# Kernel optimization log

Hardware: AMD Instinct MI355X
Metric: run time of the kernel (lower is better)

## Reference

```python
import jax, jax.numpy as jnp
import numpy as np

EPS = 1e-5
NUM_HEADS = 8
KEY_DIM = 32
V_DIM = 128  # att_ratio * key_dim

def bn2d(x, g, b, m, v):
    # inference BatchNorm2d on NCHW
    s = g * jax.lax.rsqrt(v + EPS)
    return x * s[None, :, None, None] + (b - m * s)[None, :, None, None]

def conv1x1(x, w):
    # w: [out_c, in_c], x: [B,C,H,W]
    return jnp.einsum('oc,bchw->bohw', w, x)

def _bn_params(key, c):
    k1, k2, k3, k4 = jax.random.split(key, 4)
    g = jax.random.uniform(k1, (c,), jnp.float32, 0.5, 1.5)
    b = jax.random.normal(k2, (c,), jnp.float32) * 0.1
    m = jax.random.normal(k3, (c,), jnp.float32) * 0.1
    v = jax.random.uniform(k4, (c,), jnp.float32, 0.5, 1.5)
    return g, b, m, v

def setup_inputs() -> dict:
    key = jax.random.key(0)
    ks = jax.random.split(key, 12)
    inp_dim, out_dim = 256, 512
    kv_out = (KEY_DIM + V_DIM) * NUM_HEADS      # 1280
    q_out = KEY_DIM * NUM_HEADS                 # 256
    merge_dim = V_DIM * NUM_HEADS               # 1024
    hid = out_dim * 2                            # mlp_ratio=2 -> 1024
    d = {}
    d['x'] = jax.random.normal(ks[0], (32, inp_dim, 32, 32), jnp.float32)
    d['kv_w'] = jax.random.normal(ks[1], (kv_out, inp_dim), jnp.float32) * 0.02
    d['kv_g'], d['kv_b'], d['kv_m'], d['kv_v'] = _bn_params(ks[2], kv_out)
    d['q_w'] = jax.random.normal(ks[3], (q_out, inp_dim), jnp.float32) * 0.02
    d['q_g'], d['q_b'], d['q_m'], d['q_v'] = _bn_params(ks[4], q_out)
    d['mg_w'] = jax.random.normal(ks[5], (out_dim, merge_dim), jnp.float32) * 0.02
    d['mg_g'], d['mg_b'], d['mg_m'], d['mg_v'] = _bn_params(ks[6], out_dim)
    d['fc1_w'] = jax.random.normal(ks[7], (hid, out_dim), jnp.float32) * 0.02
    d['bn1_g'], d['bn1_b'], d['bn1_m'], d['bn1_v'] = _bn_params(ks[8], hid)
    d['fc2_w'] = jax.random.normal(ks[9], (out_dim, hid), jnp.float32) * 0.02
    d['bn2_g'], d['bn2_b'], d['bn2_m'], d['bn2_v'] = _bn_params(ks[10], out_dim)
    return d

def reference(x, kv_w, kv_g, kv_b, kv_m, kv_v, q_w, q_g, q_b, q_m, q_v,
              mg_w, mg_g, mg_b, mg_m, mg_v,
              fc1_w, bn1_g, bn1_b, bn1_m, bn1_v,
              fc2_w, bn2_g, bn2_b, bn2_m, bn2_v):
    B, C, H, W = x.shape
    scale = KEY_DIM ** (-0.5)
    # kv projection: conv1x1 + BN, then split per head into k, v
    kv = bn2d(conv1x1(x, kv_w), kv_g, kv_b, kv_m, kv_v)
    kv = kv.reshape(B, NUM_HEADS, KEY_DIM + V_DIM, H * W)
    k = kv[:, :, :KEY_DIM]   # [B,h,Dk,N]
    v = kv[:, :, KEY_DIM:]   # [B,h,Dv,N]
    # query subsampling: AvgPool2d(kernel=1, stride=2) == strided slice
    xq = x[:, :, ::2, ::2]
    q = bn2d(conv1x1(xq, q_w), q_g, q_b, q_m, q_v)
    q = q.reshape(B, NUM_HEADS, KEY_DIM, -1)  # [B,h,Dk,Nq]
    # att = q^T @ k * scale, softmax over keys
    att = jax.nn.softmax(jnp.einsum('bhdq,bhdn->bhqn', q, k) * scale, axis=-1)
    h2, w2 = (H + 1) // 2, (W + 1) // 2
    # out = v @ att^T, channel-first layout
    o = jnp.einsum('bhvn,bhqn->bhvq', v, att).reshape(B, NUM_HEADS * V_DIM, h2, w2)
    # merge: GELU -> conv1x1 -> BN
    o = bn2d(conv1x1(jax.nn.gelu(o, approximate=False), mg_w), mg_g, mg_b, mg_m, mg_v)
    # ConvMlp: conv1x1 -> BN -> GELU -> conv1x1 -> BN
    y = bn2d(conv1x1(o, fc1_w), bn1_g, bn1_b, bn1_m, bn1_v)
    y = jax.nn.gelu(y, approximate=False)
    y = bn2d(conv1x1(y, fc2_w), bn2_g, bn2_b, bn2_m, bn2_v)
    return y
```

## Files before the change

kernel.cpp:

```cpp
#include <hip/hip_runtime.h>
#include <hip/hip_bf16.h>

#define BN_EPS 1e-5f

typedef short s8v __attribute__((ext_vector_type(8)));
typedef float f4v __attribute__((ext_vector_type(4)));
typedef unsigned short u16x8 __attribute__((ext_vector_type(8)));

__device__ __forceinline__ float bu2f(unsigned short u) {
    union { unsigned int i; float f; } c; c.i = ((unsigned int)u) << 16; return c.f;
}
__device__ __forceinline__ unsigned short f2bu(float f) {
    union { float f; unsigned int i; } c; c.f = f;
    unsigned int i = c.i;
    i += 0x7FFFu + ((i >> 16) & 1u);
    return (unsigned short)(i >> 16);
}
__device__ __forceinline__ float gelu_exact(float x) {
    return 0.5f * x * (1.0f + erff(x * 0.70710678118654752f));
}
__device__ __forceinline__ float ldin(const void* p, long i, bool f32) {
    return f32 ? ((const float*)p)[i] : bu2f(((const unsigned short*)p)[i]);
}
__device__ __forceinline__ s8v ldfrag(const unsigned short* p) {
    return *reinterpret_cast<const s8v*>(p);
}
__device__ __forceinline__ void gld16(const void* g, void* l) {
    __builtin_amdgcn_global_load_lds(
        (const __attribute__((address_space(1))) unsigned int*)g,
        (__attribute__((address_space(3))) unsigned int*)l, 16, 0, 0);
}
__device__ __forceinline__ s8v ldsw32(const unsigned short* T, int row, int quad) {
    return *reinterpret_cast<const s8v*>(T + row * 32 + ((quad ^ ((row >> 1) & 3)) << 3));
}
__device__ __forceinline__ s8v ldsw64(const unsigned short* T, int row, int chunk) {
    return *reinterpret_cast<const s8v*>(T + row * 64 + ((chunk ^ (row & 7)) << 3));
}
__device__ __forceinline__ int detect_f32(const unsigned short* xu) {
    int insane = 0;
    for (int i = 0; i < 128; ++i) {
        unsigned int e = (xu[i] >> 7) & 0xFFu;
        if (e == 255u || (e != 0u && (e < 96u || e > 159u))) ++insane;
    }
    return (insane >= 16) ? 1 : 0;
}

__global__ __launch_bounds__(256)
void prep_kernel(const void* __restrict__ x,
                 const void* __restrict__ w0, const void* __restrict__ w1,
                 const void* __restrict__ w2, const void* __restrict__ w3,
                 const void* __restrict__ w4,
                 unsigned short* __restrict__ wdst,
                 unsigned short* __restrict__ xT,
                 unsigned short* __restrict__ xqT,
                 int* __restrict__ dtf)
{
    __shared__ int sflag;
    __shared__ unsigned short T[64][66];
    const int tid = threadIdx.x;
    const int bid = blockIdx.x;
    if (tid == 0) {
        int fl = detect_f32((const unsigned short*)x);
        sflag = fl;
        if (bid == 0) *dtf = fl;
    }
    __syncthreads();
    const bool f = (sflag != 0);

    if (bid < 960) {
        long idx = (long)bid * 2048 + tid * 8;
        const void* s; long off;
        if (idx < 65536L) {
            long rk = idx >> 8;
            s = w0; off = ((rk >> 5) * 160 + (rk & 31)) * 256 + (idx & 255);
        } else if (idx < 327680L) {
            long rv = (idx - 65536L) >> 8;
            s = w0; off = ((rv >> 7) * 160 + 32 + (rv & 127)) * 256 + (idx & 255);
        }
        else if (idx <  393216L) { s = w1; off = idx - 327680L; }
        else if (idx <  917504L) { s = w2; off = idx - 393216L; }
        else if (idx < 1441792L) { s = w3; off = idx - 917504L; }
        else                     { s = w4; off = idx - 1441792L; }
        u16x8 pk;
        if (f) {
            float4 a = *((const float4*)((const float*)s + off));
            float4 b = *((const float4*)((const float*)s + off + 4));
            pk[0]=f2bu(a.x); pk[1]=f2bu(a.y); pk[2]=f2bu(a.z); pk[3]=f2bu(a.w);
            pk[4]=f2bu(b.x); pk[5]=f2bu(b.y); pk[6]=f2bu(b.z); pk[7]=f2bu(b.w);
        } else {
            pk = *((const u16x8*)((const unsigned short*)s + off));
        }
        *reinterpret_cast<u16x8*>(wdst + idx) = pk;
        return;
    }
    int b, c0, n0, ND; bool SUBS;
    if (bid < 3008) { int t = bid - 960;  b = t >> 6; int r = t & 63;
                      c0 = (r >> 4) * 64; n0 = (r & 15) * 64; ND = 1024; SUBS = false; }
    else            { int t = bid - 3008; b = t >> 4; int r = t & 15;
                      c0 = (r >> 2) * 64; n0 = (r & 3) * 64;  ND = 256;  SUBS = true; }
    unsigned short* dst = SUBS ? xqT : xT;
    {
        int nn = tid & 63, cq = tid >> 6;
        int n = n0 + nn;
        int sc = SUBS ? ((n >> 4) * 64 + (n & 15) * 2) : n;
        long base = ((long)b * 256 + c0 + cq * 16) * 1024 + sc;
        #pragma unroll
        for (int i = 0; i < 16; ++i)
            T[nn][cq * 16 + i] = f2bu(ldin(x, base + (long)i * 1024, f));
    }
    __syncthreads();
    {
        int cc = tid & 63, nq = tid >> 6;
        #pragma unroll
        for (int i = 0; i < 16; ++i) {
            int nn = nq * 16 + i;
            dst[((long)b * ND + n0 + nn) * 256 + c0 + cc] = T[nn][cc];
        }
    }
}

template<int OUT_MODE, bool DO_GELU, bool PRESCALE, bool REMAPK>
__global__ __launch_bounds__(256, 4)
void mfma_gemm(const unsigned short* __restrict__ A,
               const unsigned short* __restrict__ B,
               const void* __restrict__ gg, const void* __restrict__ bb,
               const void* __restrict__ mmu, const void* __restrict__ vv,
               void* __restrict__ out0,
               int M, int K, int N, const int* __restrict__ dtflag)
{
    __shared__ union {
        struct { unsigned short As[64 * 64]; unsigned short Bs[128 * 64]; } s;
        unsigned short tile[128 * 68];
    } u;
    __shared__ float sS[64], sO[64];

    const bool wf = (*dtflag != 0);
    const int tid = threadIdx.x;
    const int lane = tid & 63;
    const int wave = tid >> 6;
    const int quad = lane >> 4;
    const int l15  = lane & 15;
    const int wn2 = wave * 32;
    const int b  = blockIdx.z;
    const int bm = blockIdx.y * 64;
    const int bn = blockIdx.x * 128;

    if (tid < 64) {
        int m = bm + tid;
        int mo = REMAPK ? ((m >> 5) * 160 + (m & 31)) : m;
        float g  = ldin(gg,  mo, wf), be = ldin(bb,  mo, wf);
        float mu = ldin(mmu, mo, wf), va = ldin(vv,  mo, wf);
        float s = g * rsqrtf(va + BN_EPS);
        float o = be - mu * s;
        if (PRESCALE) { s *= 0.17677669529663687f; o *= 0.17677669529663687f; }
        sS[tid] = s; sO[tid] = o;
    }

    const unsigned short* Bb = B + (long)b * N * K;

    f4v acc[4][2];
    #pragma unroll
    for (int i = 0; i < 4; ++i)
        #pragma unroll
        for (int j = 0; j < 2; ++j) acc[i][j] = (f4v){0.f, 0.f, 0.f, 0.f};

    const int lr8 = lane >> 3;
    const int lc8 = lane & 7;

    for (int k0 = 0; k0 < K; k0 += 64) {
        #pragma unroll
        for (int j = 0; j < 2; ++j) {
            int base = wave * 16 + j * 8;
            int r = base + lr8;
            gld16(A + (long)(bm + r) * K + k0 + ((lc8 ^ (r & 7)) << 3),
                  u.s.As + base * 64);
        }
        #pragma unroll
        for (int j = 0; j < 4; ++j) {
            int base = wave * 32 + j * 8;
            int r = base + lr8;
            gld16(Bb + (long)(bn + r) * K + k0 + ((lc8 ^ (r & 7)) << 3),
                  u.s.Bs + base * 64);
        }
        __syncthreads();

        #pragma unroll
        for (int sk = 0; sk < 2; ++sk) {
            s8v af[4], bfr[2];
            #pragma unroll
            for (int i = 0; i < 4; ++i)
                af[i]  = ldsw64(u.s.As, i * 16 + l15, sk * 4 + quad);
            #pragma unroll
            for (int j = 0; j < 2; ++j)
                bfr[j] = ldsw64(u.s.Bs, wn2 + j * 16 + l15, sk * 4 + quad);
            #pragma unroll
            for (int i = 0; i < 4; ++i)
                #pragma unroll
                for (int j = 0; j < 2; ++j)
                    acc[i][j] = __builtin_amdgcn_mfma_f32_16x16x32_bf16(
                        af[i], bfr[j], acc[i][j], 0, 0, 0);
        }
        __syncthreads();
    }

    if (OUT_MODE == 0 || OUT_MODE == 3) {
        #pragma unroll
        for (int j = 0; j < 2; ++j) {
            int n = wn2 + j * 16 + l15;
            #pragma unroll
            for (int i = 0; i < 4; ++i) {
                int mcol = i * 16 + quad * 4;
                ushort4 pk;
                float v0 = acc[i][j][0] * sS[mcol + 0] + sO[mcol + 0];
                float v1 = acc[i][j][1] * sS[mcol + 1] + sO[mcol + 1];
                float v2 = acc[i][j][2] * sS[mcol + 2] + sO[mcol + 2];
                float v3 = acc[i][j][3] * sS[mcol + 3] + sO[mcol + 3];
                if (DO_GELU) {
                    v0 = gelu_exact(v0); v1 = gelu_exact(v1);
                    v2 = gelu_exact(v2); v3 = gelu_exact(v3);
                }
                pk.x = f2bu(v0); pk.y = f2bu(v1); pk.z = f2bu(v2); pk.w = f2bu(v3);
                *reinterpret_cast<ushort4*>(&u.tile[n * 68 + mcol]) = pk;
            }
        }
        __syncthreads();
        #pragma unroll
        for (int p = 0; p < 4; ++p) {
            int n = p * 32 + (tid >> 3), c = tid & 7;
            u16x8 val = *reinterpret_cast<const u16x8*>(&u.tile[n * 68 + c * 8]);
            if (OUT_MODE == 0) {
                *reinterpret_cast<u16x8*>(
                    (unsigned short*)out0 + ((long)b * N + bn + n) * M + bm + c * 8) = val;
            } else {
                int m = bm + c * 8, h = m >> 5;
                *reinterpret_cast<u16x8*>(
                    (unsigned short*)out0 + (((long)b * 8 + h) * N + bn + n) * 32 + (m & 31)) = val;
            }
        }
    } else {
        #pragma unroll
        for (int i = 0; i < 4; ++i) {
            int m0l = i * 16 + quad * 4;
            int m0  = bm + m0l;
            float s0 = sS[m0l + 0], o0 = sO[m0l + 0];
            float s1 = sS[m0l + 1], o1 = sO[m0l + 1];
            float s2 = sS[m0l + 2], o2 = sO[m0l + 2];
            float s3 = sS[m0l + 3], o3 = sO[m0l + 3];
            #pragma unroll
            for (int j = 0; j < 2; ++j) {
                int n = bn + wn2 + j * 16 + l15;
                float v0 = acc[i][j][0] * s0 + o0;
                float v1 = acc[i][j][1] * s1 + o1;
                float v2 = acc[i][j][2] * s2 + o2;
                float v3 = acc[i][j][3] * s3 + o3;
                int b2 = n >> 8, nl = n & 255;
                long ob = ((long)b2 * M + m0) * 256 + nl;
                if (wf) {
                    ((float*)out0)[ob + 0L * 256] = v0;
                    ((float*)out0)[ob + 1L * 256] = v1;
                    ((float*)out0)[ob + 2L * 256] = v2;
                    ((float*)out0)[ob + 3L * 256] = v3;
                } else {
                    ((unsigned short*)out0)[ob + 0L * 256] = f2bu(v0);
                    ((unsigned short*)out0)[ob + 1L * 256] = f2bu(v1);
                    ((unsigned short*)out0)[ob + 2L * 256] = f2bu(v2);
                    ((unsigned short*)out0)[ob + 3L * 256] = f2bu(v3);
                }
            }
        }
    }
}

__global__ __launch_bounds__(256, 4)
void kvv_gemm(const unsigned short* __restrict__ xT,
              const unsigned short* __restrict__ wV,
              const void* __restrict__ gg, const void* __restrict__ bb,
              const void* __restrict__ mmu, const void* __restrict__ vv,
              unsigned short* __restrict__ kvV, const int* __restrict__ dtflag)
{
    __shared__ union {
        struct { unsigned short As[128 * 64]; unsigned short Bs[128 * 64]; } s;
        unsigned short VT[128 * 132];
    } u;
    __shared__ float sS[128], sO[128];

    const bool wf = (*dtflag != 0);
    const int tid = threadIdx.x;
    const int lane = tid & 63;
    const int wave = tid >> 6;
    const int quad = lane >> 4;
    const int l15  = lane & 15;
    const int wm2 = (wave >> 1) * 64;
    const int wn2 = (wave & 1) * 64;
    const int b  = blockIdx.z;
    const int bv = blockIdx.x * 128;
    const int bk = blockIdx.y * 128;

    if (tid < 128) {
        int vg = bv + tid;
        int mo = (vg >> 7) * 160 + 32 + (vg & 127);
        float g  = ldin(gg,  mo, wf), be = ldin(bb,  mo, wf);
        float mu = ldin(mmu, mo, wf), va = ldin(vv,  mo, wf);
        float s = g * rsqrtf(va + BN_EPS);
        sS[tid] = s; sO[tid] = be - mu * s;
    }

    const unsigned short* Xb = xT + (long)b * 1024 * 256;

    f4v acc[4][4];
    #pragma unroll
    for (int i = 0; i < 4; ++i)
        #pragma unroll
        for (int j = 0; j < 4; ++j) acc[i][j] = (f4v){0.f, 0.f, 0.f, 0.f};

    const int lr8 = lane >> 3;
    const int lc8 = lane & 7;

    for (int k0 = 0; k0 < 256; k0 += 64) {
        #pragma unroll
        for (int j = 0; j < 4; ++j) {
            int base = wave * 32 + j * 8;
            int r = base + lr8;
            gld16(Xb + (long)(bk + r) * 256 + k0 + ((lc8 ^ (r & 7)) << 3),
                  u.s.As + base * 64);
            gld16(wV + (long)(bv + r) * 256 + k0 + ((lc8 ^ (r & 7)) << 3),
                  u.s.Bs + base * 64);
        }
        __syncthreads();

        #pragma unroll
        for (int sk = 0; sk < 2; ++sk) {
            s8v af[4], bfr[4];
            #pragma unroll
            for (int i = 0; i < 4; ++i)
                af[i]  = ldsw64(u.s.As, wm2 + i * 16 + l15, sk * 4 + quad);
            #pragma unroll
            for (int j = 0; j < 4; ++j)
                bfr[j] = ldsw64(u.s.Bs, wn2 + j * 16 + l15, sk * 4 + quad);
            #pragma unroll
            for (int i = 0; i < 4; ++i)
                #pragma unroll
                for (int j = 0; j < 4; ++j)
                    acc[i][j] = __builtin_amdgcn_mfma_f32_16x16x32_bf16(
                        af[i], bfr[j], acc[i][j], 0, 0, 0);
        }
        __syncthreads();
    }

    #pragma unroll
    for (int j = 0; j < 4; ++j) {
        int vloc = wn2 + j * 16 + l15;
        float s = sS[vloc], o = sO[vloc];
        #pragma unroll
        for (int i = 0; i < 4; ++i) {
            int kcol = wm2 + i * 16 + quad * 4;
            ushort4 pk;
            pk.x = f2bu(acc[i][j][0] * s + o);
            pk.y = f2bu(acc[i][j][1] * s + o);
            pk.z = f2bu(acc[i][j][2] * s + o);
            pk.w = f2bu(acc[i][j][3] * s + o);
            *reinterpret_cast<ushort4*>(&u.VT[vloc * 132 + kcol]) = pk;
        }
    }
    __syncthreads();
    const int h = bv >> 7;
    #pragma unroll
    for (int p = 0; p < 8; ++p) {
        int vloc = p * 16 + (tid >> 4), c = tid & 15;
        u16x8 val = *reinterpret_cast<const u16x8*>(&u.VT[vloc * 132 + c * 8]);
        *reinterpret_cast<u16x8*>(
            kvV + (((long)b * 8 + h) * 128 + (bv & 127) + vloc) * 1024 + bk + c * 8) = val;
    }
}

__global__ __launch_bounds__(512, 4)
void attn_mfma(const unsigned short* __restrict__ kvK,
               const unsigned short* __restrict__ kvV,
               const unsigned short* __restrict__ qh,
               unsigned short* __restrict__ goT)
{
    __shared__ unsigned short Ks[64 * 32];
    __shared__ unsigned short Vs[128 * 64];
    __shared__ unsigned short Ps[128][72];
    __shared__ float redS[128];

    const int tid = threadIdx.x;
    const int lane = tid & 63;
    const int wave = tid >> 6;
    const int quad = lane >> 4;
    const int l15  = lane & 15;
    const int h    = blockIdx.x;
    const int b    = blockIdx.y;
    const int q0   = blockIdx.z * 128;
    const int wq   = wave * 16;

    const unsigned short* Qb = qh  + (long)(b * 8 + h) * 256 * 32;
    const unsigned short* Kb = kvK + (long)(b * 8 + h) * 1024 * 32;
    const unsigned short* Vb = kvV + (long)(b * 8 + h) * 128 * 1024;

    s8v qf = ldfrag(Qb + (long)(q0 + wq + l15) * 32 + quad * 8);

    f4v o[8];
    #pragma unroll
    for (int i = 0; i < 8; ++i) o[i] = (f4v){0.f, 0.f, 0.f, 0.f};
    float rs[4] = {0.f, 0.f, 0.f, 0.f};

    for (int n0 = 0; n0 < 1024; n0 += 64) {
        if (wave < 4) {
            int r = wave * 16 + (lane >> 2);
            int c = (lane & 3) ^ ((r >> 1) & 3);
            gld16(Kb + (long)(n0 + r) * 32 + (c << 3), Ks + wave * 16 * 32);
        }
        {
            int rb = wave * 16;
            int r0 = rb + (lane >> 3), r1 = r0 + 8;
            int s  = lane & 7;
            gld16(Vb + (long)r0 * 1024 + n0 + ((s ^ (r0 & 7)) << 3), Vs + rb * 64);
            gld16(Vb + (long)r1 * 1024 + n0 + ((s ^ (r1 & 7)) << 3), Vs + (rb + 8) * 64);
        }
        __syncthreads();

        #pragma unroll
        for (int j = 0; j < 4; ++j) {
            s8v kf = ldsw32(Ks, j * 16 + l15, quad);
            f4v z = (f4v){0.f, 0.f, 0.f, 0.f};
            f4v sa = __builtin_amdgcn_mfma_f32_16x16x32_bf16(qf, kf, z, 0, 0, 0);
            #pragma unroll
            for (int r = 0; r < 4; ++r) {
                float p = __expf(fminf(sa[r], 30.f));
                rs[r] += p;
                Ps[wq + quad * 4 + r][j * 16 + l15] = f2bu(p);
            }
        }
        #pragma unroll
        for (int ks = 0; ks < 2; ++ks) {
            s8v pf = ldfrag(&Ps[wq + l15][ks * 32 + quad * 8]);
            #pragma unroll
            for (int i = 0; i < 8; ++i) {
                s8v vf = ldsw64(Vs, i * 16 + l15, ks * 4 + quad);
                o[i] = __builtin_amdgcn_mfma_f32_16x16x32_bf16(vf, pf, o[i], 0, 0, 0);
            }
        }
        __syncthreads();
    }

    #pragma unroll
    for (int r = 0; r < 4; ++r) {
        float s = rs[r];
        s += __shfl_xor(s, 1);
        s += __shfl_xor(s, 2);
        s += __shfl_xor(s, 4);
        s += __shfl_xor(s, 8);
        if (l15 == 0) redS[wq + quad * 4 + r] = s;
    }
    float linv = 1.0f / redS[wq + l15];
    int q = q0 + wq + l15;
    #pragma unroll
    for (int i = 0; i < 8; ++i) {
        ushort4 pk;
        pk.x = f2bu(gelu_exact(o[i][0] * linv));
        pk.y = f2bu(gelu_exact(o[i][1] * linv));
        pk.z = f2bu(gelu_exact(o[i][2] * linv));
        pk.w = f2bu(gelu_exact(o[i][3] * linv));
        *reinterpret_cast<ushort4*>(
            goT + ((long)b * 256 + q) * 1024 + h * 128 + i * 16 + quad * 4) = pk;
    }
}

extern "C" void kernel_launch(void* const* d_in, const int* in_sizes, int n_in,
                              void* d_out, int out_size, void* d_ws, size_t ws_size,
                              hipStream_t stream)
{
    const void* x     = d_in[0];
    const void* kv_w  = d_in[1];
    const void* kv_g  = d_in[2];  const void* kv_b  = d_in[3];
    const void* kv_m  = d_in[4];  const void* kv_v  = d_in[5];
    const void* q_w   = d_in[6];
    const void* q_g   = d_in[7];  const void* q_b   = d_in[8];
    const void* q_m   = d_in[9];  const void* q_v   = d_in[10];
    const void* mg_w  = d_in[11];
    const void* mg_g  = d_in[12]; const void* mg_b  = d_in[13];
    const void* mg_m  = d_in[14]; const void* mg_v  = d_in[15];
    const void* fc1_w = d_in[16];
    const void* bn1_g = d_in[17]; const void* bn1_b = d_in[18];
    const void* bn1_m = d_in[19]; const void* bn1_v = d_in[20];
    const void* fc2_w = d_in[21];
    const void* bn2_g = d_in[22]; const void* bn2_b = d_in[23];
    const void* bn2_m = d_in[24]; const void* bn2_v = d_in[25];

    unsigned short* ws  = (unsigned short*)d_ws;
    int*            dtf = (int*)d_ws;
    unsigned short* wsW  = ws + 8;
    unsigned short* wKVk = wsW;
    unsigned short* wKVv = wsW + 65536L;
    unsigned short* wQ   = wsW + 327680L;
    unsigned short* wMG  = wsW + 393216L;
    unsigned short* wFC1 = wsW + 917504L;
    unsigned short* wFC2 = wsW + 1441792L;
    unsigned short* xT   = ws + 1966088L;
    unsigned short* goT  = xT;
    unsigned short* xqT  = ws + 10354696L;
    unsigned short* qhb  = ws + 12451848L;
    unsigned short* kvK  = ws + 14549000L;
    unsigned short* kvV  = ws + 22937608L;
    unsigned short* y1T  = kvV;
    unsigned short* y2T  = kvV + 4194304L;

    dim3 blk(256, 1, 1);

    prep_kernel<<<3520, blk, 0, stream>>>(
        x, kv_w, q_w, mg_w, fc1_w, fc2_w, wsW, xT, xqT, dtf);

    mfma_gemm<3, false, true, false><<<dim3(2, 4, 32), blk, 0, stream>>>(
        wQ, xqT, q_g, q_b, q_m, q_v, qhb, 256, 256, 256, dtf);

    mfma_gemm<3, false, false, true><<<dim3(8, 4, 32), blk, 0, stream>>>(
        wKVk, xT, kv_g, kv_b, kv_m, kv_v, kvK, 256, 256, 1024, dtf);

    kvv_gemm<<<dim3(8, 8, 32), blk, 0, stream>>>(
        xT, wKVv, kv_g, kv_b, kv_m, kv_v, kvV, dtf);

    attn_mfma<<<dim3(8, 32, 2), dim3(512, 1, 1), 0, stream>>>(kvK, kvV, qhb, goT);

    mfma_gemm<0, false, false, false><<<dim3(64, 8, 1), blk, 0, stream>>>(
        wMG, goT, mg_g, mg_b, mg_m, mg_v, y1T, 512, 1024, 8192, dtf);

    mfma_gemm<0, true, false, false><<<dim3(64, 16, 1), blk, 0, stream>>>(
        wFC1, y1T, bn1_g, bn1_b, bn1_m, bn1_v, y2T, 1024, 512, 8192, dtf);

    mfma_gemm<2, false, false, false><<<dim3(64, 8, 1), blk, 0, stream>>>(
        wFC2, y2T, bn2_g, bn2_b, bn2_m, bn2_v, d_out, 512, 1024, 8192, dtf);
}
```

Baseline: 316.7 us.

## Double-buffer LDS tiles in GEMM and attention, transpose score MFMA, stage fp32 epilogue

Adds double-buffered shared-memory staging to the generic MFMA GEMM and the attention kernel, so the next K/V or A/B tile loads while the current one is computed, with one barrier per iteration. The attention score MFMA is transposed so each lane holds four keys of one query. This allows packed 64-bit P stores and a row-sum reduction done with two shuffles instead of a shared-memory reduction. The fp32 GEMM epilogue now goes through an LDS tile to emit coalesced float4 stores, and optional GELU is added. Doubling the buffers raises LDS use per block, which may lower occupancy.

```diff
diff --git a/kernel.cpp b/kernel.cpp
--- a/kernel.cpp
+++ b/kernel.cpp
@@ -129,8 +129,9 @@
                int M, int K, int N, const int* __restrict__ dtflag)
 {
     __shared__ union {
-        struct { unsigned short As[64 * 64]; unsigned short Bs[128 * 64]; } s;
+        struct { unsigned short As[2][64 * 64]; unsigned short Bs[2][128 * 64]; } s;
         unsigned short tile[128 * 68];
+        float ftile[64 * 132];
     } u;
     __shared__ float sS[64], sO[64];
 
@@ -167,32 +168,38 @@
     const int lr8 = lane >> 3;
     const int lc8 = lane & 7;
 
-    for (int k0 = 0; k0 < K; k0 += 64) {
+    auto stage = [&](int k0, int bufi) {
         #pragma unroll
         for (int j = 0; j < 2; ++j) {
             int base = wave * 16 + j * 8;
             int r = base + lr8;
             gld16(A + (long)(bm + r) * K + k0 + ((lc8 ^ (r & 7)) << 3),
-                  u.s.As + base * 64);
+                  u.s.As[bufi] + base * 64);
         }
         #pragma unroll
         for (int j = 0; j < 4; ++j) {
             int base = wave * 32 + j * 8;
             int r = base + lr8;
             gld16(Bb + (long)(bn + r) * K + k0 + ((lc8 ^ (r & 7)) << 3),
-                  u.s.Bs + base * 64);
-        }
-        __syncthreads();
-
+                  u.s.Bs[bufi] + base * 64);
+        }
+    };
+
+    stage(0, 0);
+    __syncthreads();
+
+    for (int k0 = 0; k0 < K; k0 += 64) {
+        int cur = (k0 >> 6) & 1;
+        if (k0 + 64 < K) stage(k0 + 64, cur ^ 1);
         #pragma unroll
         for (int sk = 0; sk < 2; ++sk) {
             s8v af[4], bfr[2];
             #pragma unroll
             for (int i = 0; i < 4; ++i)
-                af[i]  = ldsw64(u.s.As, i * 16 + l15, sk * 4 + quad);
+                af[i]  = ldsw64(u.s.As[cur], i * 16 + l15, sk * 4 + quad);
             #pragma unroll
             for (int j = 0; j < 2; ++j)
-                bfr[j] = ldsw64(u.s.Bs, wn2 + j * 16 + l15, sk * 4 + quad);
+                bfr[j] = ldsw64(u.s.Bs[cur], wn2 + j * 16 + l15, sk * 4 + quad);
             #pragma unroll
             for (int i = 0; i < 4; ++i)
                 #pragma unroll
@@ -238,33 +245,47 @@
             }
         }
     } else {
-        #pragma unroll
-        for (int i = 0; i < 4; ++i) {
-            int m0l = i * 16 + quad * 4;
-            int m0  = bm + m0l;
-            float s0 = sS[m0l + 0], o0 = sO[m0l + 0];
-            float s1 = sS[m0l + 1], o1 = sO[m0l + 1];
-            float s2 = sS[m0l + 2], o2 = sO[m0l + 2];
-            float s3 = sS[m0l + 3], o3 = sO[m0l + 3];
-            #pragma unroll
-            for (int j = 0; j < 2; ++j) {
-                int n = bn + wn2 + j * 16 + l15;
-                float v0 = acc[i][j][0] * s0 + o0;
-                float v1 = acc[i][j][1] * s1 + o1;
-                float v2 = acc[i][j][2] * s2 + o2;
-                float v3 = acc[i][j][3] * s3 + o3;
-                int b2 = n >> 8, nl = n & 255;
-                long ob = ((long)b2 * M + m0) * 256 + nl;
-                if (wf) {
-                    ((float*)out0)[ob + 0L * 256] = v0;
-                    ((float*)out0)[ob + 1L * 256] = v1;
-                    ((float*)out0)[ob + 2L * 256] = v2;
-                    ((float*)out0)[ob + 3L * 256] = v3;
-                } else {
-                    ((unsigned short*)out0)[ob + 0L * 256] = f2bu(v0);
-                    ((unsigned short*)out0)[ob + 1L * 256] = f2bu(v1);
-                    ((unsigned short*)out0)[ob + 2L * 256] = f2bu(v2);
-                    ((unsigned short*)out0)[ob + 3L * 256] = f2bu(v3);
+        if (wf) {
+            #pragma unroll
+            for (int i = 0; i < 4; ++i) {
+                int m0l = i * 16 + quad * 4;
+                #pragma unroll
+                for (int j = 0; j < 2; ++j) {
+                    int n = wn2 + j * 16 + l15;
+                    #pragma unroll
+                    for (int r = 0; r < 4; ++r) {
+                        float v = acc[i][j][r] * sS[m0l + r] + sO[m0l + r];
+                        if (DO_GELU) v = gelu_exact(v);
+                        u.ftile[(m0l + r) * 132 + n] = v;
+                    }
+                }
+            }
+            __syncthreads();
+            int b2 = bn >> 8;
+            #pragma unroll
+            for (int p = 0; p < 8; ++p) {
+                int m = p * 8 + (tid >> 5);
+                int c = (tid & 31) * 4;
+                float4 val = *reinterpret_cast<const float4*>(&u.ftile[m * 132 + c]);
+                *reinterpret_cast<float4*>(
+                    (float*)out0 + ((long)b2 * M + bm + m) * 256 + (bn & 255) + c) = val;
+            }
+        } else {
+            #pragma unroll
+            for (int i = 0; i < 4; ++i) {
+                int m0l = i * 16 + quad * 4;
+                int m0  = bm + m0l;
+                #pragma unroll
+                for (int j = 0; j < 2; ++j) {
+                    int n = bn + wn2 + j * 16 + l15;
+                    int b2 = n >> 8, nl = n & 255;
+                    long ob = ((long)b2 * M + m0) * 256 + nl;
+                    #pragma unroll
+                    for (int r = 0; r < 4; ++r) {
+                        float v = acc[i][j][r] * sS[m0l + r] + sO[m0l + r];
+                        if (DO_GELU) v = gelu_exact(v);
+                        ((unsigned short*)out0)[ob + (long)r * 256] = f2bu(v);
+                    }
                 }
             }
         }
@@ -379,10 +400,9 @@
                const unsigned short* __restrict__ qh,
                unsigned short* __restrict__ goT)
 {
-    __shared__ unsigned short Ks[64 * 32];
-    __shared__ unsigned short Vs[128 * 64];
+    __shared__ unsigned short Ks[2][64 * 32];
+    __shared__ unsigned short Vs[2][128 * 64];
     __shared__ unsigned short Ps[128][72];
-    __shared__ float redS[128];
 
     const int tid = threadIdx.x;
     const int lane = tid & 63;
@@ -403,57 +423,59 @@
     f4v o[8];
     #pragma unroll
     for (int i = 0; i < 8; ++i) o[i] = (f4v){0.f, 0.f, 0.f, 0.f};
-    float rs[4] = {0.f, 0.f, 0.f, 0.f};
-
-    for (int n0 = 0; n0 < 1024; n0 += 64) {
+    float rsum = 0.f;
+
+    auto stage = [&](int n0, int bufi) {
         if (wave < 4) {
             int r = wave * 16 + (lane >> 2);
             int c = (lane & 3) ^ ((r >> 1) & 3);
-            gld16(Kb + (long)(n0 + r) * 32 + (c << 3), Ks + wave * 16 * 32);
-        }
-        {
-            int rb = wave * 16;
-            int r0 = rb + (lane >> 3), r1 = r0 + 8;
-            int s  = lane & 7;
-            gld16(Vb + (long)r0 * 1024 + n0 + ((s ^ (r0 & 7)) << 3), Vs + rb * 64);
-            gld16(Vb + (long)r1 * 1024 + n0 + ((s ^ (r1 & 7)) << 3), Vs + (rb + 8) * 64);
-        }
-        __syncthreads();
+            gld16(Kb + (long)(n0 + r) * 32 + (c << 3), Ks[bufi] + wave * 16 * 32);
+        }
+        int rb = wave * 16;
+        int r0 = rb + (lane >> 3), r1 = r0 + 8;
+        int s  = lane & 7;
+        gld16(Vb + (long)r0 * 1024 + n0 + ((s ^ (r0 & 7)) << 3), Vs[bufi] + rb * 64);
+        gld16(Vb + (long)r1 * 1024 + n0 + ((s ^ (r1 & 7)) << 3), Vs[bufi] + (rb + 8) * 64);
+    };
+
+    stage(0, 0);
+    __syncthreads();
+
+    for (int n0 = 0; n0 < 1024; n0 += 64) {
+        int cur = (n0 >> 6) & 1;
+        if (n0 + 64 < 1024) stage(n0 + 64, cur ^ 1);
 
         #pragma unroll
         for (int j = 0; j < 4; ++j) {
-            s8v kf = ldsw32(Ks, j * 16 + l15, quad);
+            s8v kf = ldsw32(Ks[cur], j * 16 + l15, quad);
             f4v z = (f4v){0.f, 0.f, 0.f, 0.f};
-            f4v sa = __builtin_amdgcn_mfma_f32_16x16x32_bf16(qf, kf, z, 0, 0, 0);
-            #pragma unroll
-            for (int r = 0; r < 4; ++r) {
-                float p = __expf(fminf(sa[r], 30.f));
-                rs[r] += p;
-                Ps[wq + quad * 4 + r][j * 16 + l15] = f2bu(p);
-            }
+            f4v st = __builtin_amdgcn_mfma_f32_16x16x32_bf16(kf, qf, z, 0, 0, 0);
+            float p0 = __expf(fminf(st[0], 30.f));
+            float p1 = __expf(fminf(st[1], 30.f));
+            float p2 = __expf(fminf(st[2], 30.f));
+            float p3 = __expf(fminf(st[3], 30.f));
+            rsum += (p0 + p1) + (p2 + p3);
+            unsigned int lo = (unsigned)f2bu(p0) | ((unsigned)f2bu(p1) << 16);
+            unsigned int hi = (unsigned)f2bu(p2) | ((unsigned)f2bu(p3) << 16);
+            *reinterpret_cast<uint2*>(&Ps[wq + l15][j * 16 + quad * 4]) =
+                make_uint2(lo, hi);
         }
         #pragma unroll
         for (int ks = 0; ks < 2; ++ks) {
             s8v pf = ldfrag(&Ps[wq + l15][ks * 32 + quad * 8]);
             #pragma unroll
             for (int i = 0; i < 8; ++i) {
-                s8v vf = ldsw64(Vs, i * 16 + l15, ks * 4 + quad);
+                s8v vf = ldsw64(Vs[cur], i * 16 + l15, ks * 4 + quad);
                 o[i] = __builtin_amdgcn_mfma_f32_16x16x32_bf16(vf, pf, o[i], 0, 0, 0);
             }
         }
         __syncthreads();
     }
 
-    #pragma unroll
-    for (int r = 0; r < 4; ++r) {
-        float s = rs[r];
-        s += __shfl_xor(s, 1);
-        s += __shfl_xor(s, 2);
-        s += __shfl_xor(s, 4);
-        s += __shfl_xor(s, 8);
-        if (l15 == 0) redS[wq + quad * 4 + r] = s;
-    }
-    float linv = 1.0f / redS[wq + l15];
+    rsum += __shfl_xor(rsum, 16);
+    rsum += __shfl_xor(rsum, 32);
+    float linv = 1.0f / rsum;
+
     int q = q0 + wq + l15;
     #pragma unroll
     for (int i = 0; i < 8; ++i) {
```

Result: slower. 326.3 us (+3.0%).
